# Optimization experiments

Measured on AMD Instinct MI355X. Metric: run time of the kernel, lower is better.

Reference implementation:

```python
import jax, jax.numpy as jnp
import numpy as np

DIM = 1024
B, S = 16, 2048

def setup_inputs() -> dict:
    key = jax.random.key(0)
    ks = jax.random.split(key, 8)
    scale = 1.0 / np.sqrt(DIM)
    x = jax.random.normal(ks[0], (B, S, DIM), dtype=jnp.float32)
    mask = jax.random.randint(ks[1], (B, S), 0, 2, dtype=jnp.int32)
    Wq = jax.random.normal(ks[2], (DIM, DIM), dtype=jnp.float32) * scale
    Wk = jax.random.normal(ks[3], (DIM, DIM), dtype=jnp.float32) * scale
    Wv = jax.random.normal(ks[4], (DIM, DIM), dtype=jnp.float32) * scale
    bq = jax.random.normal(ks[5], (DIM,), dtype=jnp.float32) * 0.01
    bk = jax.random.normal(ks[6], (DIM,), dtype=jnp.float32) * 0.01
    bv = jax.random.normal(ks[7], (DIM,), dtype=jnp.float32) * 0.01
    return {"x": x, "mask": mask, "Wq": Wq, "bq": bq, "Wk": Wk, "bk": bk, "Wv": Wv, "bv": bv}

def reference(x, mask, Wq, bq, Wk, bk, Wv, bv):
    # Q/K/V projections (torch Linear: x @ W.T + b)
    Q = jnp.einsum('bsd,ed->bse', x, Wq) + bq
    K = jnp.einsum('bsd,ed->bse', x, Wk) + bk
    V = jnp.einsum('bsd,ed->bse', x, Wv) + bv
    inv_sqrt_d = 1.0 / jnp.sqrt(jnp.asarray(x.shape[-1], dtype=x.dtype))
    scores = jnp.einsum('bqd,bkd->bqk', Q, K) * inv_sqrt_d  # [B,S,S]
    # mask: [B,S] -> broadcast over query dim; 0 = padding -> -inf
    scores = jnp.where(mask[:, None, :] == 0, -jnp.inf, scores)
    attn = jax.nn.softmax(scores, axis=-1)
    attn = jnp.nan_to_num(attn, nan=0.0)  # rows fully masked -> 0 (matches torch)
    out = jnp.einsum('bqk,bkd->bqd', attn, V)
    return out.mean(axis=1)  # [B, DIM]
```

## Files before the change

### kernel.cpp

```cpp
#include <hip/hip_runtime.h>
#include <hip/hip_bf16.h>
#include <stdint.h>

#define NBATCH 16
#define SEQ    2048
#define DMODEL 1024
#define KSPLIT 16

#define CS      0.03125f
#define KSC     3.0517578125e-5f
#define NEG4LN2 2.772588722f

typedef __attribute__((ext_vector_type(8))) short short8;
typedef __attribute__((ext_vector_type(4))) float f32x4;
typedef __attribute__((ext_vector_type(4))) int i32x4;
typedef __attribute__((ext_vector_type(16))) int i32x16;

struct __align__(8) bf4 { __hip_bfloat16 h[4]; };

__device__ __forceinline__ float bf2f(short s) {
  union { uint32_t u; float f; } c;
  c.u = ((uint32_t)(uint16_t)s) << 16;
  return c.f;
}
__device__ __forceinline__ int qs8(float f, float sc) {
  int v = __float2int_rn(f * sc);
  return v > 127 ? 127 : (v < -127 ? -127 : v);
}

__device__ __forceinline__ void gload16(const void* g, void* l) {
  __builtin_amdgcn_global_load_lds(
      (const __attribute__((address_space(1))) void*)g,
      (__attribute__((address_space(3))) void*)l, 16, 0, 0);
}

#define BAR() __builtin_amdgcn_s_barrier()
#define WAIT_LGKM0()                                         \
  do {                                                       \
    asm volatile("s_waitcnt lgkmcnt(0)" ::: "memory");       \
    __builtin_amdgcn_sched_barrier(0);                       \
  } while (0)
#define WAIT_VM0()                                           \
  do {                                                       \
    asm volatile("s_waitcnt vmcnt(0)" ::: "memory");         \
  } while (0)

template <int TP>
__global__ __launch_bounds__(512, 2)
void gemmT_kernel(const __hip_bfloat16* __restrict__ Aall,
                  const __hip_bfloat16* __restrict__ Ball,
                  uint8_t* __restrict__ O8, int ldo) {
  __shared__ __align__(16) char smem[131072];
  const int t = threadIdx.x, lane = t & 63, wid = t >> 6;
  const int wm = wid >> 2, wn = wid & 3;
  const int g = lane >> 4, l15 = lane & 15, l7 = lane & 7;

  const int at2base = blockIdx.x * TP;
  const int bt2 = blockIdx.y;
  const __hip_bfloat16* Bb = Ball + (size_t)bt2 * 256 * DMODEL;
  auto Aof = [&](int tp) { return Aall + (size_t)(at2base + tp) * 256 * DMODEL; };

  const int srl = t >> 3;
  const int sc8 = (t & 7) ^ (srl & 7);
  const int pc8[2] = {g ^ l7, (4 + g) ^ l7};

  auto stage_mat = [&](const __hip_bfloat16* gs, char* dst, int kt) {
#pragma unroll
    for (int it = 0; it < 4; ++it)
      gload16(gs + (size_t)(it * 64 + srl) * DMODEL + kt * 64 + sc8 * 8,
              dst + it * 8192 + wid * 1024);
  };

  f32x4 acc[8][4];
#pragma unroll
  for (int m = 0; m < 8; ++m)
#pragma unroll
    for (int n = 0; n < 4; ++n) acc[m][n] = (f32x4){0.f, 0.f, 0.f, 0.f};
  short8 afr[2][4], bfr[2][2][2];

#define LDA_Q(MH)                                                           \
  { _Pragma("unroll") for (int m = 0; m < 4; ++m) {                         \
      const int row = wm * 128 + ((MH) * 4 + m) * 16 + l15;                 \
      afr[0][m] = *(const short8*)(At + row * 128 + pc8[0] * 16);           \
      afr[1][m] = *(const short8*)(At + row * 128 + pc8[1] * 16);           \
    } }
#define LDB_Q(NH)                                                           \
  { _Pragma("unroll") for (int n = 0; n < 2; ++n) {                         \
      const int row = wn * 64 + ((NH) * 2 + n) * 16 + l15;                  \
      bfr[NH][0][n] = *(const short8*)(Bt + row * 128 + pc8[0] * 16);       \
      bfr[NH][1][n] = *(const short8*)(Bt + row * 128 + pc8[1] * 16);       \
    } }
#define MFMA_Q(MH, NH)                                                      \
  { __builtin_amdgcn_s_setprio(1);                                          \
    _Pragma("unroll") for (int kk = 0; kk < 2; ++kk)                        \
    _Pragma("unroll") for (int m = 0; m < 4; ++m)                           \
    _Pragma("unroll") for (int n = 0; n < 2; ++n)                           \
      acc[(MH)*4+m][(NH)*2+n] = __builtin_amdgcn_mfma_f32_16x16x32_bf16(    \
          afr[kk][m], bfr[NH][kk][n], acc[(MH)*4+m][(NH)*2+n], 0, 0, 0);    \
    __builtin_amdgcn_s_setprio(0); }

  auto EPI = [&](int at2) {
    const size_t orow0 = (size_t)bt2 * 256 + wn * 64 + l15;
    const int ocol0 = at2 * 256 + wm * 128 + g * 4;
#pragma unroll
    for (int mi = 0; mi < 8; ++mi)
#pragma unroll
      for (int ni = 0; ni < 4; ++ni) {
        uint32_t pk = 0;
#pragma unroll
        for (int j = 0; j < 4; ++j)
          pk |= (uint32_t)(qs8(acc[mi][ni][j], 1024.f) & 0xff) << (8 * j);
        *(uint32_t*)(O8 + (orow0 + ni * 16) * (size_t)ldo + ocol0 + mi * 16) = pk;
      }
#pragma unroll
    for (int m = 0; m < 8; ++m)
#pragma unroll
      for (int n = 0; n < 4; ++n) acc[m][n] = (f32x4){0.f, 0.f, 0.f, 0.f};
  };

  stage_mat(Aof(0), smem, 0);
  stage_mat(Bb, smem + 32768, 0);
  WAIT_VM0();
  BAR();

  const int NI = 16 * TP;
#pragma unroll 1
  for (int ii = 0; ii < NI; ++ii) {
    const int p = ii & 1;
    const char* At = smem + (p << 16);
    const char* Bt = smem + 32768 + (p << 16);
    char* An = smem + ((p ^ 1) << 16);
    char* Bn = smem + 32768 + ((p ^ 1) << 16);
    const int kn = (ii + 1) & 15;
    LDA_Q(0) LDB_Q(0)
    if (ii + 1 < NI) stage_mat(Aof((ii + 1) >> 4), An, kn);
    BAR(); WAIT_LGKM0(); MFMA_Q(0, 0) BAR();
    LDB_Q(1)
    if (ii + 1 < NI) stage_mat(Bb, Bn, kn);
    BAR(); WAIT_LGKM0(); MFMA_Q(0, 1) BAR();
    LDA_Q(1)
    BAR(); WAIT_LGKM0(); MFMA_Q(1, 0) BAR();
    MFMA_Q(1, 1)
    WAIT_VM0();
    if ((ii & 15) == 15) EPI(at2base + (ii >> 4));
    BAR();
  }
#undef LDA_Q
#undef LDB_Q
#undef MFMA_Q
}

template <int MODE, int TP>
__global__ __launch_bounds__(512, 2)
void i8gemm_kernel(const uint8_t* __restrict__ Aall,
                   const uint8_t* __restrict__ Ball,
                   uint8_t* __restrict__ OUT8,
                   const float* __restrict__ vball,
                   float* __restrict__ Zpart, int b0) {
  __shared__ __align__(16) char smem[131072 + 2048];
  const int t = threadIdx.x, lane = t & 63, wid = t >> 6;
  const int wm = wid >> 2, wn = wid & 3;
  const int l31 = lane & 31, half = lane >> 5, l7 = lane & 7;

  int at2base, bt2, cb = 0, b = 0;
  const uint8_t *Bb, *Abatch;
  if constexpr (MODE == 0) {
    at2base = blockIdx.x * TP;
    bt2 = blockIdx.y;
    Abatch = Aall;
    Bb = Ball + (size_t)bt2 * 256 * DMODEL;
  } else {
    cb = blockIdx.y; b = b0 + cb;
    bt2 = blockIdx.x & 7;
    at2base = (blockIdx.x >> 3) * TP;
    Abatch = Aall + (size_t)b * SEQ * DMODEL;
    Bb = Ball + ((size_t)b * SEQ + bt2 * 256) * DMODEL;
  }
  auto Aof = [&](int tp) { return Abatch + (size_t)(at2base + tp) * 256 * DMODEL; };

  const int srl = t >> 3;
  const int sc8 = (t & 7) ^ (srl & 7);
  int pcI[4];
#pragma unroll
  for (int ks = 0; ks < 4; ++ks) pcI[ks] = ((ks * 2 + half) ^ l7) * 16;

  auto stage8 = [&](const uint8_t* gs, char* dst, int kt) {
#pragma unroll
    for (int it = 0; it < 4; ++it)
      gload16(gs + (size_t)(it * 64 + srl) * DMODEL + kt * 128 + sc8 * 16,
              dst + it * 8192 + wid * 1024);
  };

  i32x16 acci[4][2];
#pragma unroll
  for (int m = 0; m < 4; ++m)
#pragma unroll
    for (int n = 0; n < 2; ++n)
#pragma unroll
      for (int r = 0; r < 16; ++r) acci[m][n][r] = 0;
  i32x4 afr[2][4], bfr[2][4];

  const int rowA0 = wm * 128 + l31;
  const int rowB0 = wn * 64 + l31;

#define LDA_I(MH)                                                           \
  { _Pragma("unroll") for (int mm = 0; mm < 2; ++mm) {                      \
      const int rb = (rowA0 + ((MH) * 2 + mm) * 32) * 128;                  \
      _Pragma("unroll") for (int ks = 0; ks < 4; ++ks)                      \
        afr[mm][ks] = *(const i32x4*)(At + rb + pcI[ks]);                   \
    } }
#define LDB_I(NH)                                                           \
  { const int rb = (rowB0 + (NH) * 32) * 128;                               \
    _Pragma("unroll") for (int ks = 0; ks < 4; ++ks)                        \
      bfr[NH][ks] = *(const i32x4*)(Bt + rb + pcI[ks]); }
#define MFMA_I(MH, NH)                                                      \
  { __builtin_amdgcn_s_setprio(1);                                          \
    _Pragma("unroll") for (int ks = 0; ks < 4; ++ks)                        \
    _Pragma("unroll") for (int mm = 0; mm < 2; ++mm)                        \
      acci[(MH)*2+mm][NH] = __builtin_amdgcn_mfma_i32_32x32x32_i8(          \
          afr[mm][ks], bfr[NH][ks], acci[(MH)*2+mm][NH], 0, 0, 0);          \
    __builtin_amdgcn_s_setprio(0); }

  auto EPI = [&](int at2) {
    if constexpr (MODE == 0) {
      const int bcol0 = bt2 * 256 + wn * 64 + l31;
#pragma unroll
      for (int m = 0; m < 4; ++m) {
        const int arow_base = at2 * 256 + wm * 128 + m * 32 + 4 * half;
#pragma unroll
        for (int n = 0; n < 2; ++n) {
          const int bcol = bcol0 + n * 32;
#pragma unroll
          for (int r = 0; r < 16; ++r) {
            const int arow = arow_base + (r & 3) + 8 * (r >> 2);
            OUT8[(size_t)arow * DMODEL + bcol] =
                (uint8_t)qs8((float)acci[m][n][r], 9.765625e-4f);
          }
        }
      }
    } else {
      float zc[2] = {0.f, 0.f};
      const int qcol0 = bt2 * 256 + wn * 64 + l31;
#pragma unroll
      for (int m = 0; m < 4; ++m) {
        const int krow_base = at2 * 256 + wm * 128 + m * 32 + 4 * half;
        float4 vv[4];
#pragma unroll
        for (int gg = 0; gg < 4; ++gg)
          vv[gg] = *(const float4*)&vball[(size_t)b * SEQ + krow_base + 8 * gg];
#pragma unroll
        for (int n = 0; n < 2; ++n) {
          const int qcol = qcol0 + n * 32;
#pragma unroll
          for (int r = 0; r < 16; r += 2) {
            const float vj0 = ((const float*)&vv[r >> 2])[r & 3];
            const float vj1 = ((const float*)&vv[r >> 2])[(r + 1) & 3];
            const float e0 = __expf(fmaf((float)acci[m][n][r], KSC, vj0));
            const float e1 = __expf(fmaf((float)acci[m][n][r + 1], KSC, vj1));
            zc[n] += e0 + e1;
            const unsigned p = __builtin_amdgcn_cvt_pk_fp8_f32(e0, e1, 0, false);
            const int krow = krow_base + (r & 3) + 8 * (r >> 2);
            uint8_t* ad = OUT8 + ((size_t)cb * SEQ + krow) * (size_t)SEQ + qcol;
            ad[0] = (uint8_t)p;
            ad[SEQ] = (uint8_t)(p >> 8);
          }
        }
      }
#pragma unroll
      for (int n = 0; n < 2; ++n) {
        float v = zc[n];
        v += __shfl_xor(v, 32);
        zc[n] = v;
      }
      float* red = (float*)(smem + 131072);
      if (lane < 32) {
#pragma unroll
        for (int n = 0; n < 2; ++n)
          red[wm * 256 + wn * 64 + n * 32 + l31] = zc[n];
      }
      __syncthreads();
      if (t < 256)
        Zpart[((size_t)cb * 8 + at2) * SEQ + bt2 * 256 + t] = red[t] + red[256 + t];
    }
#pragma unroll
    for (int m = 0; m < 4; ++m)
#pragma unroll
      for (int n = 0; n < 2; ++n)
#pragma unroll
        for (int r = 0; r < 16; ++r) acci[m][n][r] = 0;
  };

  stage8(Aof(0), smem, 0);
  stage8(Bb, smem + 32768, 0);
  WAIT_VM0();
  BAR();

  const int NI = 8 * TP;
#pragma unroll 1
  for (int ii = 0; ii < NI; ++ii) {
    const int p = ii & 1;
    const char* At = smem + (p << 16);
    const char* Bt = smem + 32768 + (p << 16);
    char* An = smem + ((p ^ 1) << 16);
    char* Bn = smem + 32768 + ((p ^ 1) << 16);
    const int kn = (ii + 1) & 7;
    LDA_I(0) LDB_I(0)
    if (ii + 1 < NI) stage8(Aof((ii + 1) >> 3), An, kn);
    BAR(); WAIT_LGKM0(); MFMA_I(0, 0) BAR();
    LDB_I(1)
    if (ii + 1 < NI) stage8(Bb, Bn, kn);
    BAR(); WAIT_LGKM0(); MFMA_I(0, 1) BAR();
    LDA_I(1)
    BAR(); WAIT_LGKM0(); MFMA_I(1, 0) BAR();
    MFMA_I(1, 1)
    WAIT_VM0();
    if ((ii & 7) == 7) EPI(at2base + (ii >> 3));
    BAR();
  }
#undef LDA_I
#undef LDB_I
#undef MFMA_I
}

__global__ void transpose_cvt_kernel(const float* __restrict__ in,
                                     __hip_bfloat16* __restrict__ outp) {
  __shared__ float tile[32][33];
  const int bx = blockIdx.x, by = blockIdx.y;
  const int tx = threadIdx.x & 31, ty = threadIdx.x >> 5;
#pragma unroll
  for (int r = 0; r < 32; r += 8)
    tile[ty + r][tx] = in[(size_t)(by * 32 + ty + r) * DMODEL + bx * 32 + tx];
  __syncthreads();
#pragma unroll
  for (int r = 0; r < 32; r += 8)
    outp[(size_t)(bx * 32 + ty + r) * DMODEL + by * 32 + tx] =
        __float2bfloat16(tile[tx][ty + r]);
}

__global__ __launch_bounds__(256)
void prep_t2_kernel(const __hip_bfloat16* __restrict__ WkT,
                    const float* __restrict__ bq, float* __restrict__ t2) {
  const int wave = threadIdx.x >> 6, lane = threadIdx.x & 63;
  const int d = blockIdx.x * 4 + wave;
  const short8* kr = (const short8*)(WkT + (size_t)d * DMODEL);
  float a2 = 0.f;
#pragma unroll
  for (int h = 0; h < 2; ++h) {
    const short8 kv = kr[lane * 2 + h];
    const int e0 = lane * 16 + h * 8;
#pragma unroll
    for (int i = 0; i < 8; ++i) a2 += bf2f(kv[i]) * bq[e0 + i];
  }
  a2 += __shfl_down(a2, 32); a2 += __shfl_down(a2, 16); a2 += __shfl_down(a2, 8);
  a2 += __shfl_down(a2, 4);  a2 += __shfl_down(a2, 2);  a2 += __shfl_down(a2, 1);
  if (lane == 0) t2[d] = a2;
}

__global__ __launch_bounds__(256)
void cvtv_kernel(const float* __restrict__ x, const float* __restrict__ t2,
                 const int* __restrict__ mask,
                 uint8_t* __restrict__ x8, float* __restrict__ vb) {
  const int wave = threadIdx.x >> 6, lane = threadIdx.x & 63;
  const size_t row = (size_t)blockIdx.x * 4 + wave;
  const float* xr = x + row * DMODEL;
  float a2 = 0.f;
#pragma unroll
  for (int p = 0; p < 4; ++p) {
    const int d = p * 256 + lane * 4;
    const float4 xv = *(const float4*)(xr + d);
    const float4 tv = *(const float4*)(t2 + d);
    a2 += xv.x * tv.x + xv.y * tv.y + xv.z * tv.z + xv.w * tv.w;
    uint32_t qp = (uint32_t)(qs8(xv.x, 32.f) & 0xff) |
                  ((uint32_t)(qs8(xv.y, 32.f) & 0xff) << 8) |
                  ((uint32_t)(qs8(xv.z, 32.f) & 0xff) << 16) |
                  ((uint32_t)(qs8(xv.w, 32.f) & 0xff) << 24);
    *(uint32_t*)(x8 + row * DMODEL + d) = qp;
  }
  a2 += __shfl_down(a2, 32); a2 += __shfl_down(a2, 16); a2 += __shfl_down(a2, 8);
  a2 += __shfl_down(a2, 4);  a2 += __shfl_down(a2, 2);  a2 += __shfl_down(a2, 1);
  if (lane == 0)
    vb[row] = mask[row] ? fmaf(a2, CS, -NEG4LN2) : -1e30f;
}

__global__ void zinv_kernel(const float* __restrict__ Zpart,
                            float* __restrict__ rZ, int n) {
  const int idx = blockIdx.x * 256 + threadIdx.x;
  if (idx >= n) return;
  const int cb = idx >> 11, q = idx & (SEQ - 1);
  float z = 0.f;
#pragma unroll
  for (int kt = 0; kt < 8; ++kt)
    z += Zpart[((size_t)cb * 8 + kt) * SEQ + q];
  rZ[(size_t)cb * SEQ + q] = (z > 0.f) ? (1.f / z) : 0.f;
}

__global__ __launch_bounds__(256)
void passB_kernel(const uint8_t* __restrict__ E8,
                  const float* __restrict__ rZ,
                  float* __restrict__ wout) {
  const int t = threadIdx.x, lane = t & 63, wave = t >> 6;
  const int cb = blockIdx.y;
  float4 rzv[4][2];
#pragma unroll
  for (int it = 0; it < 4; ++it) {
    const float4* p = (const float4*)(rZ + (size_t)cb * SEQ + it * 512 + lane * 8);
    rzv[it][0] = p[0];
    rzv[it][1] = p[1];
  }
  const int kbase = blockIdx.x * 16 + wave * 4;
#pragma unroll
  for (int r = 0; r < 4; ++r) {
    const int k = kbase + r;
    const uint2* Ep = (const uint2*)(E8 + ((size_t)cb * SEQ + k) * SEQ);
    float s = 0.f;
#pragma unroll
    for (int it = 0; it < 4; ++it) {
      const uint2 v = Ep[it * 64 + lane];
      const float* rz = (const float*)&rzv[it][0];
      s += __builtin_amdgcn_cvt_f32_fp8(v.x, 0) * rz[0];
      s += __builtin_amdgcn_cvt_f32_fp8(v.x, 1) * rz[1];
      s += __builtin_amdgcn_cvt_f32_fp8(v.x, 2) * rz[2];
      s += __builtin_amdgcn_cvt_f32_fp8(v.x, 3) * rz[3];
      s += __builtin_amdgcn_cvt_f32_fp8(v.y, 0) * rz[4];
      s += __builtin_amdgcn_cvt_f32_fp8(v.y, 1) * rz[5];
      s += __builtin_amdgcn_cvt_f32_fp8(v.y, 2) * rz[6];
      s += __builtin_amdgcn_cvt_f32_fp8(v.y, 3) * rz[7];
    }
    s += __shfl_down(s, 32); s += __shfl_down(s, 16); s += __shfl_down(s, 8);
    s += __shfl_down(s, 4);  s += __shfl_down(s, 2);  s += __shfl_down(s, 1);
    if (lane == 0) wout[(size_t)cb * SEQ + k] = s;
  }
}

__global__ void sumw_kernel(const float* __restrict__ w,
                            float* __restrict__ sumw_all, int b0) {
  __shared__ float sred[4];
  const int t = threadIdx.x, lane = t & 63, wave = t >> 6;
  const int cb = blockIdx.x;
  float v = 0.f;
  for (int k = t; k < SEQ; k += 256) v += w[(size_t)cb * SEQ + k];
  v += __shfl_down(v, 32); v += __shfl_down(v, 16); v += __shfl_down(v, 8);
  v += __shfl_down(v, 4);  v += __shfl_down(v, 2);  v += __shfl_down(v, 1);
  if (lane == 0) sred[wave] = v;
  __syncthreads();
  if (t == 0) sumw_all[b0 + cb] = sred[0] + sred[1] + sred[2] + sred[3];
}

__global__ __launch_bounds__(256)
void wxpart_kernel(const uint8_t* __restrict__ x8,
                   const float* __restrict__ w,
                   float* __restrict__ wxp, int b0) {
  const int cb = blockIdx.y, kq = blockIdx.z;
  const int b = b0 + cb;
  const int d4 = threadIdx.x;
  const uint8_t* xb =
      x8 + ((size_t)b * SEQ + (size_t)kq * (SEQ / KSPLIT)) * DMODEL;
  const float* wb = w + (size_t)cb * SEQ + (size_t)kq * (SEQ / KSPLIT);
  float a0 = 0.f, a1 = 0.f, a2 = 0.f, a3 = 0.f;
#pragma unroll 4
  for (int k = 0; k < SEQ / KSPLIT; ++k) {
    const float wk = wb[k];
    const uint32_t pv = *(const uint32_t*)(xb + (size_t)k * DMODEL + d4 * 4);
    a0 += wk * (float)(int8_t)(pv & 0xff);
    a1 += wk * (float)(int8_t)((pv >> 8) & 0xff);
    a2 += wk * (float)(int8_t)((pv >> 16) & 0xff);
    a3 += wk * (float)(int8_t)(pv >> 24);
  }
  float4* o = (float4*)&wxp[((size_t)kq * NBATCH + b) * DMODEL + d4 * 4];
  *o = make_float4(a0 * 0.03125f, a1 * 0.03125f, a2 * 0.03125f, a3 * 0.03125f);
}

__global__ void final_kernel(const float* __restrict__ wxp,
                             const float* __restrict__ sumw_all,
                             const float* __restrict__ Wv,
                             const float* __restrict__ bv,
                             float* __restrict__ out) {
  const int b = blockIdx.y, eg = blockIdx.x;
  const int wave = threadIdx.x >> 6, lane = threadIdx.x & 63;
  const int e = eg * 4 + wave;
  float acc = 0.f;
  for (int d = lane; d < DMODEL; d += 64) {
    float wx = 0.f;
#pragma unroll
    for (int kq = 0; kq < KSPLIT; ++kq)
      wx += wxp[((size_t)kq * NBATCH + b) * DMODEL + d];
    acc += wx * Wv[(size_t)e * DMODEL + d];
  }
  acc += __shfl_down(acc, 32); acc += __shfl_down(acc, 16);
  acc += __shfl_down(acc, 8);  acc += __shfl_down(acc, 4);
  acc += __shfl_down(acc, 2);  acc += __shfl_down(acc, 1);
  if (lane == 0)
    out[(size_t)b * DMODEL + e] =
        (acc + sumw_all[b] * bv[e]) * (1.f / (float)SEQ);
}

extern "C" void kernel_launch(void* const* d_in, const int* in_sizes, int n_in,
                              void* d_out, int out_size, void* d_ws, size_t ws_size,
                              hipStream_t stream) {
  const float* x  = (const float*)d_in[0];
  const int* mask = (const int*)d_in[1];
  const float* Wq = (const float*)d_in[2];
  const float* bq = (const float*)d_in[3];
  const float* Wk = (const float*)d_in[4];
  const float* bk = (const float*)d_in[5];
  const float* Wv = (const float*)d_in[6];
  const float* bv = (const float*)d_in[7];
  float* out = (float*)d_out;
  (void)bk;

  char* ws = (char*)d_ws;
  size_t off = 0;
  auto alloc = [&](size_t bytes) -> void* {
    void* p = ws + off;
    off += (bytes + 255) & ~(size_t)255;
    return p;
  };
  uint8_t* Mt8 = (uint8_t*)alloc((size_t)DMODEL * DMODEL);
  __hip_bfloat16* WqT_bf = (__hip_bfloat16*)alloc((size_t)DMODEL * DMODEL * 2);
  __hip_bfloat16* WkT_bf = (__hip_bfloat16*)alloc((size_t)DMODEL * DMODEL * 2);
  float* wxp      = (float*)alloc((size_t)KSPLIT * NBATCH * DMODEL * 4);
  float* sumw_all = (float*)alloc((size_t)NBATCH * 4);
  float* t2       = (float*)alloc((size_t)DMODEL * 4);
  uint8_t* x8i = (uint8_t*)alloc((size_t)NBATCH * SEQ * DMODEL);
  uint8_t* Y8i = (uint8_t*)alloc((size_t)NBATCH * SEQ * DMODEL);
  float* vb = (float*)alloc((size_t)NBATCH * SEQ * 4);
  const size_t fixed = off;

  const size_t per_batch = (size_t)SEQ * SEQ
                         + (size_t)8 * SEQ * 4
                         + (size_t)2 * SEQ * 4 + 8 * 256;
  long avail = (long)ws_size - (long)fixed;
  int NB = (int)(avail / (long)per_batch);
  if (NB < 1) NB = 1;
  if (NB > NBATCH) NB = NBATCH;
  while (NBATCH % NB) --NB;
  uint8_t* Ebuf = (uint8_t*)alloc((size_t)NB * SEQ * SEQ);
  float* Zpart = (float*)alloc((size_t)NB * 8 * SEQ * 4);
  float* rZ    = (float*)alloc((size_t)NB * SEQ * 4);
  float* wbuf  = (float*)alloc((size_t)NB * SEQ * 4);

  transpose_cvt_kernel<<<dim3(32, 32), dim3(256), 0, stream>>>(Wq, WqT_bf);
  transpose_cvt_kernel<<<dim3(32, 32), dim3(256), 0, stream>>>(Wk, WkT_bf);
  gemmT_kernel<1><<<dim3(4, 4), dim3(512), 0, stream>>>(
      WqT_bf, WkT_bf, Mt8, DMODEL);
  prep_t2_kernel<<<dim3(256), dim3(256), 0, stream>>>(WkT_bf, bq, t2);
  cvtv_kernel<<<dim3(NBATCH * SEQ / 4), dim3(256), 0, stream>>>(
      x, t2, mask, x8i, vb);
  i8gemm_kernel<0, 2><<<dim3(NBATCH * SEQ / 512, DMODEL / 256), dim3(512), 0,
                        stream>>>(x8i, Mt8, Y8i, nullptr, nullptr, 0);

  for (int b0 = 0; b0 < NBATCH; b0 += NB) {
    const int nb = NB;
    i8gemm_kernel<1, 4><<<dim3(16, nb), dim3(512), 0, stream>>>(
        x8i, Y8i, Ebuf, vb, Zpart, b0);
    zinv_kernel<<<dim3((nb * SEQ + 255) / 256), dim3(256), 0, stream>>>(
        Zpart, rZ, nb * SEQ);
    passB_kernel<<<dim3(SEQ / 16, nb), dim3(256), 0, stream>>>(Ebuf, rZ, wbuf);
    sumw_kernel<<<dim3(nb), dim3(256), 0, stream>>>(wbuf, sumw_all, b0);
    wxpart_kernel<<<dim3(1, nb, KSPLIT), dim3(256), 0, stream>>>(
        x8i, wbuf, wxp, b0);
  }
  final_kernel<<<dim3(DMODEL / 4, NBATCH), dim3(256), 0, stream>>>(
      wxp, sumw_all, Wv, bv, out);
}
```

Measured before the change: 274.3 us.

## Shrink int8 GEMM tiles to 256x128 with K=64 steps for higher occupancy

```diff
diff --git a/kernel.cpp b/kernel.cpp
--- a/kernel.cpp
+++ b/kernel.cpp
@@ -151,113 +151,88 @@
 }
 
 template <int MODE, int TP>
-__global__ __launch_bounds__(512, 2)
+__global__ __launch_bounds__(512, 4)
 void i8gemm_kernel(const uint8_t* __restrict__ Aall,
                    const uint8_t* __restrict__ Ball,
                    uint8_t* __restrict__ OUT8,
                    const float* __restrict__ vball,
                    float* __restrict__ Zpart, int b0) {
-  __shared__ __align__(16) char smem[131072 + 2048];
+  __shared__ __align__(16) char smem[49152 + 2048];
   const int t = threadIdx.x, lane = t & 63, wid = t >> 6;
-  const int wm = wid >> 2, wn = wid & 3;
-  const int l31 = lane & 31, half = lane >> 5, l7 = lane & 7;
-
-  int at2base, bt2, cb = 0, b = 0;
+  const int wm = wid >> 1, wn = wid & 1;
+  const int l31 = lane & 31, half = lane >> 5;
+
+  int at2base, bt2, cb = 0, b = 0, qt = 0;
   const uint8_t *Bb, *Abatch;
   if constexpr (MODE == 0) {
     at2base = blockIdx.x * TP;
     bt2 = blockIdx.y;
     Abatch = Aall;
-    Bb = Ball + (size_t)bt2 * 256 * DMODEL;
+    Bb = Ball + (size_t)bt2 * 128 * DMODEL;
   } else {
     cb = blockIdx.y; b = b0 + cb;
-    bt2 = blockIdx.x & 7;
-    at2base = (blockIdx.x >> 3) * TP;
+    qt = blockIdx.x & 15;
+    at2base = (blockIdx.x >> 4) * TP;
     Abatch = Aall + (size_t)b * SEQ * DMODEL;
-    Bb = Ball + ((size_t)b * SEQ + bt2 * 256) * DMODEL;
+    Bb = Ball + ((size_t)b * SEQ + qt * 128) * DMODEL;
   }
   auto Aof = [&](int tp) { return Abatch + (size_t)(at2base + tp) * 256 * DMODEL; };
 
-  const int srl = t >> 3;
-  const int sc8 = (t & 7) ^ (srl & 7);
-  int pcI[4];
-#pragma unroll
-  for (int ks = 0; ks < 4; ++ks) pcI[ks] = ((ks * 2 + half) ^ l7) * 16;
-
-  auto stage8 = [&](const uint8_t* gs, char* dst, int kt) {
-#pragma unroll
-    for (int it = 0; it < 4; ++it)
-      gload16(gs + (size_t)(it * 64 + srl) * DMODEL + kt * 128 + sc8 * 16,
-              dst + it * 8192 + wid * 1024);
+  auto stageA = [&](const uint8_t* gs, char* dst, int kt) {
+#pragma unroll
+    for (int j = 0; j < 2; ++j) {
+      const int slot = t + j * 512;
+      gload16(gs + (size_t)(slot & 255) * DMODEL + kt * 64 + (slot >> 8) * 16,
+              dst + j * 8192 + wid * 1024);
+    }
   };
-
-  i32x16 acci[4][2];
-#pragma unroll
-  for (int m = 0; m < 4; ++m)
+  auto stageB = [&](const uint8_t* gs, char* dst, int kt) {
+    gload16(gs + (size_t)(t & 127) * DMODEL + kt * 64 + (t >> 7) * 16,
+            dst + wid * 1024);
+  };
+
+  i32x16 acci[2][2];
+#pragma unroll
+  for (int m = 0; m < 2; ++m)
 #pragma unroll
     for (int n = 0; n < 2; ++n)
 #pragma unroll
       for (int r = 0; r < 16; ++r) acci[m][n][r] = 0;
-  i32x4 afr[2][4], bfr[2][4];
-
-  const int rowA0 = wm * 128 + l31;
-  const int rowB0 = wn * 64 + l31;
-
-#define LDA_I(MH)                                                           \
-  { _Pragma("unroll") for (int mm = 0; mm < 2; ++mm) {                      \
-      const int rb = (rowA0 + ((MH) * 2 + mm) * 32) * 128;                  \
-      _Pragma("unroll") for (int ks = 0; ks < 4; ++ks)                      \
-        afr[mm][ks] = *(const i32x4*)(At + rb + pcI[ks]);                   \
-    } }
-#define LDB_I(NH)                                                           \
-  { const int rb = (rowB0 + (NH) * 32) * 128;                               \
-    _Pragma("unroll") for (int ks = 0; ks < 4; ++ks)                        \
-      bfr[NH][ks] = *(const i32x4*)(Bt + rb + pcI[ks]); }
-#define MFMA_I(MH, NH)                                                      \
-  { __builtin_amdgcn_s_setprio(1);                                          \
-    _Pragma("unroll") for (int ks = 0; ks < 4; ++ks)                        \
-    _Pragma("unroll") for (int mm = 0; mm < 2; ++mm)                        \
-      acci[(MH)*2+mm][NH] = __builtin_amdgcn_mfma_i32_32x32x32_i8(          \
-          afr[mm][ks], bfr[NH][ks], acci[(MH)*2+mm][NH], 0, 0, 0);          \
-    __builtin_amdgcn_s_setprio(0); }
 
   auto EPI = [&](int at2) {
     if constexpr (MODE == 0) {
-      const int bcol0 = bt2 * 256 + wn * 64 + l31;
-#pragma unroll
-      for (int m = 0; m < 4; ++m) {
-        const int arow_base = at2 * 256 + wm * 128 + m * 32 + 4 * half;
-#pragma unroll
-        for (int n = 0; n < 2; ++n) {
-          const int bcol = bcol0 + n * 32;
+      const int bcol0 = bt2 * 128 + wn * 64 + l31;
+#pragma unroll
+      for (int mt = 0; mt < 2; ++mt) {
+        const int arow_base = at2 * 256 + wm * 64 + mt * 32 + 4 * half;
+#pragma unroll
+        for (int nt = 0; nt < 2; ++nt)
 #pragma unroll
           for (int r = 0; r < 16; ++r) {
             const int arow = arow_base + (r & 3) + 8 * (r >> 2);
-            OUT8[(size_t)arow * DMODEL + bcol] =
-                (uint8_t)qs8((float)acci[m][n][r], 9.765625e-4f);
+            OUT8[(size_t)arow * DMODEL + bcol0 + nt * 32] =
+                (uint8_t)qs8((float)acci[mt][nt][r], 9.765625e-4f);
           }
-        }
       }
     } else {
       float zc[2] = {0.f, 0.f};
-      const int qcol0 = bt2 * 256 + wn * 64 + l31;
-#pragma unroll
-      for (int m = 0; m < 4; ++m) {
-        const int krow_base = at2 * 256 + wm * 128 + m * 32 + 4 * half;
+#pragma unroll
+      for (int mt = 0; mt < 2; ++mt) {
+        const int krow_base = at2 * 256 + wm * 64 + mt * 32 + 4 * half;
         float4 vv[4];
 #pragma unroll
         for (int gg = 0; gg < 4; ++gg)
           vv[gg] = *(const float4*)&vball[(size_t)b * SEQ + krow_base + 8 * gg];
 #pragma unroll
-        for (int n = 0; n < 2; ++n) {
-          const int qcol = qcol0 + n * 32;
+        for (int nt = 0; nt < 2; ++nt) {
+          const int qcol = qt * 128 + wn * 64 + nt * 32 + l31;
 #pragma unroll
           for (int r = 0; r < 16; r += 2) {
             const float vj0 = ((const float*)&vv[r >> 2])[r & 3];
             const float vj1 = ((const float*)&vv[r >> 2])[(r + 1) & 3];
-            const float e0 = __expf(fmaf((float)acci[m][n][r], KSC, vj0));
-            const float e1 = __expf(fmaf((float)acci[m][n][r + 1], KSC, vj1));
-            zc[n] += e0 + e1;
+            const float e0 = __expf(fmaf((float)acci[mt][nt][r], KSC, vj0));
+            const float e1 = __expf(fmaf((float)acci[mt][nt][r + 1], KSC, vj1));
+            zc[nt] += e0 + e1;
             const unsigned p = __builtin_amdgcn_cvt_pk_fp8_f32(e0, e1, 0, false);
             const int krow = krow_base + (r & 3) + 8 * (r >> 2);
             uint8_t* ad = OUT8 + ((size_t)cb * SEQ + krow) * (size_t)SEQ + qcol;
@@ -267,59 +242,71 @@
         }
       }
 #pragma unroll
-      for (int n = 0; n < 2; ++n) {
-        float v = zc[n];
+      for (int nt = 0; nt < 2; ++nt) {
+        float v = zc[nt];
         v += __shfl_xor(v, 32);
-        zc[n] = v;
+        zc[nt] = v;
       }
-      float* red = (float*)(smem + 131072);
+      float* red = (float*)(smem + 49152);
       if (lane < 32) {
 #pragma unroll
-        for (int n = 0; n < 2; ++n)
-          red[wm * 256 + wn * 64 + n * 32 + l31] = zc[n];
+        for (int nt = 0; nt < 2; ++nt)
+          red[wm * 128 + wn * 64 + nt * 32 + l31] = zc[nt];
       }
       __syncthreads();
-      if (t < 256)
-        Zpart[((size_t)cb * 8 + at2) * SEQ + bt2 * 256 + t] = red[t] + red[256 + t];
+      if (t < 128)
+        Zpart[((size_t)cb * 8 + at2) * SEQ + qt * 128 + t] =
+            red[t] + red[128 + t] + red[256 + t] + red[384 + t];
     }
 #pragma unroll
-    for (int m = 0; m < 4; ++m)
+    for (int m = 0; m < 2; ++m)
 #pragma unroll
       for (int n = 0; n < 2; ++n)
 #pragma unroll
         for (int r = 0; r < 16; ++r) acci[m][n][r] = 0;
   };
 
-  stage8(Aof(0), smem, 0);
-  stage8(Bb, smem + 32768, 0);
+  stageA(Aof(0), smem, 0);
+  stageB(Bb, smem + 16384, 0);
   WAIT_VM0();
   BAR();
 
-  const int NI = 8 * TP;
+  const int NI = 16 * TP;
 #pragma unroll 1
   for (int ii = 0; ii < NI; ++ii) {
     const int p = ii & 1;
-    const char* At = smem + (p << 16);
-    const char* Bt = smem + 32768 + (p << 16);
-    char* An = smem + ((p ^ 1) << 16);
-    char* Bn = smem + 32768 + ((p ^ 1) << 16);
-    const int kn = (ii + 1) & 7;
-    LDA_I(0) LDB_I(0)
-    if (ii + 1 < NI) stage8(Aof((ii + 1) >> 3), An, kn);
-    BAR(); WAIT_LGKM0(); MFMA_I(0, 0) BAR();
-    LDB_I(1)
-    if (ii + 1 < NI) stage8(Bb, Bn, kn);
-    BAR(); WAIT_LGKM0(); MFMA_I(0, 1) BAR();
-    LDA_I(1)
-    BAR(); WAIT_LGKM0(); MFMA_I(1, 0) BAR();
-    MFMA_I(1, 1)
+    const char* Al = smem + p * 24576;
+    const char* Bl = smem + 16384 + p * 24576;
+    i32x4 af[2][2], bf[2][2];
+#pragma unroll
+    for (int ks = 0; ks < 2; ++ks) {
+      const int s4 = ks * 2 + half;
+#pragma unroll
+      for (int mt = 0; mt < 2; ++mt)
+        af[mt][ks] = *(const i32x4*)(Al + s4 * 4096 + (wm * 64 + mt * 32 + l31) * 16);
+#pragma unroll
+      for (int nt = 0; nt < 2; ++nt)
+        bf[nt][ks] = *(const i32x4*)(Bl + s4 * 2048 + (wn * 64 + nt * 32 + l31) * 16);
+    }
+    if (ii + 1 < NI) {
+      stageA(Aof((ii + 1) >> 4), smem + (p ^ 1) * 24576, (ii + 1) & 15);
+      stageB(Bb, smem + 16384 + (p ^ 1) * 24576, (ii + 1) & 15);
+    }
+    WAIT_LGKM0();
+    __builtin_amdgcn_s_setprio(1);
+#pragma unroll
+    for (int ks = 0; ks < 2; ++ks)
+#pragma unroll
+      for (int mt = 0; mt < 2; ++mt)
+#pragma unroll
+        for (int nt = 0; nt < 2; ++nt)
+          acci[mt][nt] = __builtin_amdgcn_mfma_i32_32x32x32_i8(
+              af[mt][ks], bf[nt][ks], acci[mt][nt], 0, 0, 0);
+    __builtin_amdgcn_s_setprio(0);
     WAIT_VM0();
-    if ((ii & 7) == 7) EPI(at2base + (ii >> 3));
+    if ((ii & 15) == 15) EPI(at2base + (ii >> 4));
     BAR();
   }
-#undef LDA_I
-#undef LDB_I
-#undef MFMA_I
 }
 
 __global__ void transpose_cvt_kernel(const float* __restrict__ in,
@@ -546,12 +533,12 @@
   prep_t2_kernel<<<dim3(256), dim3(256), 0, stream>>>(WkT_bf, bq, t2);
   cvtv_kernel<<<dim3(NBATCH * SEQ / 4), dim3(256), 0, stream>>>(
       x, t2, mask, x8i, vb);
-  i8gemm_kernel<0, 2><<<dim3(NBATCH * SEQ / 512, DMODEL / 256), dim3(512), 0,
-                        stream>>>(x8i, Mt8, Y8i, nullptr, nullptr, 0);
+  i8gemm_kernel<0, 2><<<dim3(64, DMODEL / 128), dim3(512), 0, stream>>>(
+      x8i, Mt8, Y8i, nullptr, nullptr, 0);
 
   for (int b0 = 0; b0 < NBATCH; b0 += NB) {
     const int nb = NB;
-    i8gemm_kernel<1, 4><<<dim3(16, nb), dim3(512), 0, stream>>>(
+    i8gemm_kernel<1, 4><<<dim3(32, nb), dim3(512), 0, stream>>>(
         x8i, Y8i, Ebuf, vb, Zpart, b0);
     zinv_kernel<<<dim3((nb * SEQ + 255) / 256), dim3(256), 0, stream>>>(
         Zpart, rZ, nb * SEQ);
```

After: 361.9 us. 1.32x slower.
